# Kernel tuning notes

Measured on AMD Instinct MI355X. Metric: run time of the kernel, lower is better.

The kernel has to match this reference:

```python
import jax, jax.numpy as jnp
import numpy as np

INPUT_SIZE, HIDDEN, LEVELS = 64, 256, 2
T, B = 2048, 128


def _lstm_layer(x_seq, h0, c0, W_ih, W_hh, b_ih, b_hh):
    """Run one LSTM layer over the full sequence. x_seq: [T,B,D] -> hs: [T,B,H].
    PyTorch gate order: i, f, g, o."""
    def step(carry, x_t):
        h, c = carry
        z = x_t @ W_ih.T + b_ih + h @ W_hh.T + b_hh  # [B, 4H]
        i, f, g, o = jnp.split(z, 4, axis=-1)
        i = jax.nn.sigmoid(i)
        f = jax.nn.sigmoid(f)
        g = jnp.tanh(g)
        o = jax.nn.sigmoid(o)
        c = f * c + i * g
        h = o * jnp.tanh(c)
        return (h, c), h
    _, hs = jax.lax.scan(step, (h0, c0), x_seq)
    return hs


def setup_inputs() -> dict:
    key = jax.random.key(0)
    ks = jax.random.split(key, 16)
    s = 1.0 / np.sqrt(HIDDEN)
    inp = {
        "x": jax.random.normal(ks[0], (T, B, INPUT_SIZE), dtype=jnp.float32),
        "h0": jax.random.uniform(ks[1], (LEVELS, B, HIDDEN), dtype=jnp.float32),
        "c0": jax.random.uniform(ks[2], (LEVELS, B, HIDDEN), dtype=jnp.float32),
        # layer 0 (input -> hidden)
        "W_ih0": jax.random.uniform(ks[3], (4 * HIDDEN, INPUT_SIZE), jnp.float32, -s, s),
        "W_hh0": jax.random.uniform(ks[4], (4 * HIDDEN, HIDDEN), jnp.float32, -s, s),
        "b_ih0": jax.random.uniform(ks[5], (4 * HIDDEN,), jnp.float32, -s, s),
        "b_hh0": jax.random.uniform(ks[6], (4 * HIDDEN,), jnp.float32, -s, s),
        # layer 1 (hidden -> hidden)
        "W_ih1": jax.random.uniform(ks[7], (4 * HIDDEN, HIDDEN), jnp.float32, -s, s),
        "W_hh1": jax.random.uniform(ks[8], (4 * HIDDEN, HIDDEN), jnp.float32, -s, s),
        "b_ih1": jax.random.uniform(ks[9], (4 * HIDDEN,), jnp.float32, -s, s),
        "b_hh1": jax.random.uniform(ks[10], (4 * HIDDEN,), jnp.float32, -s, s),
        # linear head hidden -> 1
        "W_lin": jax.random.uniform(ks[11], (1, HIDDEN), jnp.float32, -s, s),
        "b_lin": jax.random.uniform(ks[12], (1,), jnp.float32, -s, s),
    }
    return inp


def reference(x, h0, c0, W_ih0, W_hh0, b_ih0, b_hh0, W_ih1, W_hh1, b_ih1, b_hh1, W_lin, b_lin):
    hs0 = _lstm_layer(x, h0[0], c0[0], W_ih0, W_hh0, b_ih0, b_hh0)   # [T,B,H]
    hs1 = _lstm_layer(hs0, h0[1], c0[1], W_ih1, W_hh1, b_ih1, b_hh1)  # [T,B,H]
    out = hs1 @ W_lin.T + b_lin  # [T,B,1]
    return out[..., 0]  # [T,B] (matches torch stack().squeeze())
```

## Files before the change

### kernel.cpp

```cpp
#include <hip/hip_runtime.h>

constexpr int TT   = 2048;
constexpr int NB   = 128;
constexpr int NI   = 64;
constexpr int NH   = 256;
constexpr int NGRP = 128;
constexpr int NWG  = 256;
constexpr int NTHR = 512;
constexpr int R0   = 8;
constexpr int R1   = 16;
constexpr int HLAG = 8;
constexpr int SLOT = (NH / 2) * NB;

__device__ unsigned g_c[64];
__device__ unsigned g_cnt = 0, g_gen = 0;

__device__ __forceinline__ float sigm(float v) { return 1.0f / (1.0f + __expf(-v)); }
__device__ __forceinline__ float tanhfast(float v) {
    float e = __expf(2.0f * v);
    return 1.0f - 2.0f / (e + 1.0f);
}
__device__ __forceinline__ float asfl(unsigned u) { return __uint_as_float(u); }
__device__ __forceinline__ unsigned f2bf(float f) {
    unsigned u = __float_as_uint(f);
    return (u + 0x7fffu + ((u >> 16) & 1u)) >> 16;
}

__device__ __forceinline__ unsigned long long ldq(const unsigned* p) {
    return __hip_atomic_load((const unsigned long long*)p, __ATOMIC_RELAXED,
                             __HIP_MEMORY_SCOPE_AGENT);
}
__device__ __forceinline__ unsigned ldd(const unsigned* p) {
    return __hip_atomic_load(p, __ATOMIC_RELAXED, __HIP_MEMORY_SCOPE_AGENT);
}
__device__ __forceinline__ void std_(unsigned* p, unsigned v) {
    __hip_atomic_store(p, v, __ATOMIC_RELAXED, __HIP_MEMORY_SCOPE_AGENT);
}
__device__ __forceinline__ void bump(unsigned* p) {
    (void)__hip_atomic_fetch_add(p, 1u, __ATOMIC_RELAXED, __HIP_MEMORY_SCOPE_AGENT);
}

__device__ __forceinline__ void pollboth(unsigned n0, unsigned n1, int lane) {
    const unsigned* p = &g_c[(lane & 1) * 32];
    for (;;) {
        unsigned v = ldd(p);
        unsigned c0v = (unsigned)__shfl((int)v, 0);
        unsigned c1v = (unsigned)__shfl((int)v, 1);
        if (c0v >= n0 && c1v >= n1) return;
        __builtin_amdgcn_s_sleep(1);
    }
}

__device__ __forceinline__ void gridbar(unsigned k, bool last) {
    __syncthreads();
    if (threadIdx.x == 0) {
        __threadfence();
        unsigned a = __hip_atomic_fetch_add(&g_cnt, 1u, __ATOMIC_ACQ_REL,
                                            __HIP_MEMORY_SCOPE_AGENT);
        if (a == k * NWG - 1u) {
            if (last) {
                __hip_atomic_store(&g_cnt, 0u, __ATOMIC_RELAXED, __HIP_MEMORY_SCOPE_AGENT);
                __hip_atomic_store(&g_gen, 0u, __ATOMIC_RELEASE, __HIP_MEMORY_SCOPE_AGENT);
            } else {
                __hip_atomic_store(&g_gen, k, __ATOMIC_RELEASE, __HIP_MEMORY_SCOPE_AGENT);
            }
        } else if (!last) {
            while (__hip_atomic_load(&g_gen, __ATOMIC_RELAXED,
                                     __HIP_MEMORY_SCOPE_AGENT) < k)
                __builtin_amdgcn_s_sleep(1);
        }
        __threadfence();
    }
    __syncthreads();
}

#define STEPQ(Q, HA, HB)                                   \
    acc[0]  += w00.Q * (HA); acc[1]  += w00.Q * (HB);      \
    acc[2]  += w01.Q * (HA); acc[3]  += w01.Q * (HB);      \
    acc[4]  += w02.Q * (HA); acc[5]  += w02.Q * (HB);      \
    acc[6]  += w03.Q * (HA); acc[7]  += w03.Q * (HB);      \
    acc[8]  += w10.Q * (HA); acc[9]  += w10.Q * (HB);      \
    acc[10] += w11.Q * (HA); acc[11] += w11.Q * (HB);      \
    acc[12] += w12.Q * (HA); acc[13] += w12.Q * (HB);      \
    acc[14] += w13.Q * (HA); acc[15] += w13.Q * (HB);

#define LOADW(W, K, kk)                                                        \
    float4 w00 = *(const float4*)((W) + (size_t)(0 * NH + j0    ) * (K) + (kk)); \
    float4 w01 = *(const float4*)((W) + (size_t)(1 * NH + j0    ) * (K) + (kk)); \
    float4 w02 = *(const float4*)((W) + (size_t)(2 * NH + j0    ) * (K) + (kk)); \
    float4 w03 = *(const float4*)((W) + (size_t)(3 * NH + j0    ) * (K) + (kk)); \
    float4 w10 = *(const float4*)((W) + (size_t)(0 * NH + j0 + 1) * (K) + (kk)); \
    float4 w11 = *(const float4*)((W) + (size_t)(1 * NH + j0 + 1) * (K) + (kk)); \
    float4 w12 = *(const float4*)((W) + (size_t)(2 * NH + j0 + 1) * (K) + (kk)); \
    float4 w13 = *(const float4*)((W) + (size_t)(3 * NH + j0 + 1) * (K) + (kk));

__device__ __forceinline__ void partH_bf(const float* __restrict__ W, int j0,
                                         int kbase,
                                         const unsigned* __restrict__ hd,
                                         int lane, float* acc) {
    const unsigned* hp = hd + (size_t)(kbase >> 1) * NB + (lane << 1);
    #pragma unroll 4
    for (int i = 0; i < 16; ++i) {
        const int kk = kbase + (i << 2);
        LOADW(W, NH, kk)
        unsigned long long q0 = ldq(hp + (size_t)(2 * i) * NB);
        unsigned long long q1 = ldq(hp + (size_t)(2 * i + 1) * NB);
        unsigned d00 = (unsigned)q0, d01 = (unsigned)(q0 >> 32);
        unsigned d10 = (unsigned)q1, d11 = (unsigned)(q1 >> 32);
        STEPQ(x, asfl(d00 << 16),          asfl(d01 << 16))
        STEPQ(y, asfl(d00 & 0xffff0000u),  asfl(d01 & 0xffff0000u))
        STEPQ(z, asfl(d10 << 16),          asfl(d11 << 16))
        STEPQ(w, asfl(d10 & 0xffff0000u),  asfl(d11 & 0xffff0000u))
    }
}

__device__ __forceinline__ void partX(const float* __restrict__ W, int j0,
                                      int k0, const float* __restrict__ xp,
                                      int lane, float* acc) {
    #pragma unroll
    for (int i4 = 0; i4 < 4; ++i4) {
        const int kk = k0 + (i4 << 2);
        LOADW(W, NI, kk)
        float4 xa = *(const float4*)(xp + (size_t)(lane << 1) * NI + kk);
        float4 xb = *(const float4*)(xp + (size_t)((lane << 1) + 1) * NI + kk);
        STEPQ(x, xa.x, xb.x)
        STEPQ(y, xa.y, xb.y)
        STEPQ(z, xa.z, xb.z)
        STEPQ(w, xa.w, xb.w)
    }
}

__global__ void __launch_bounds__(NTHR, 2) lstm2(
    const float* __restrict__ x,
    const float* __restrict__ h0in, const float* __restrict__ c0in,
    const float* __restrict__ Wih0, const float* __restrict__ Whh0,
    const float* __restrict__ bih0, const float* __restrict__ bhh0,
    const float* __restrict__ Wih1, const float* __restrict__ Whh1,
    const float* __restrict__ bih1, const float* __restrict__ bhh1,
    const float* __restrict__ Wlin, const float* __restrict__ blin,
    float* __restrict__ out,
    unsigned* __restrict__ h0d, unsigned* __restrict__ h1d)
{
    __shared__ __align__(16) float4 zp4[16 * NB];
    __shared__ float red[4];
    __shared__ unsigned go_w;

    const int tid  = threadIdx.x;
    const int gid  = blockIdx.x;
    const bool is1 = gid >= NGRP;
    const int g    = is1 ? gid - NGRP : gid;
    const int j0   = g * 2;
    const int lane = tid & 63;
    const int wv   = __builtin_amdgcn_readfirstlane(tid >> 6);

    unsigned* ownc   = is1 ? &g_c[32] : &g_c[0];

    float4 bsA = make_float4(0, 0, 0, 0), bsB = bsA;
    float cA = 0.f, cB = 0.f;
    if (tid < 128) {
        const float* bi = is1 ? bih1 : bih0;
        const float* bh = is1 ? bhh1 : bhh0;
        bsA.x = bi[0 * NH + j0] + bh[0 * NH + j0];
        bsA.y = bi[1 * NH + j0] + bh[1 * NH + j0];
        bsA.z = bi[2 * NH + j0] + bh[2 * NH + j0];
        bsA.w = bi[3 * NH + j0] + bh[3 * NH + j0];
        bsB.x = bi[0 * NH + j0 + 1] + bh[0 * NH + j0 + 1];
        bsB.y = bi[1 * NH + j0 + 1] + bh[1 * NH + j0 + 1];
        bsB.z = bi[2 * NH + j0 + 1] + bh[2 * NH + j0 + 1];
        bsB.w = bi[3 * NH + j0 + 1] + bh[3 * NH + j0 + 1];
        const float* cbase = c0in + (is1 ? 1 : 0) * NB * NH + (size_t)tid * NH + j0;
        cA = cbase[0]; cB = cbase[1];
        const float* hbase = h0in + (is1 ? 1 : 0) * NB * NH + (size_t)tid * NH + j0;
        unsigned d = (f2bf(hbase[1]) << 16) | f2bf(hbase[0]);
        unsigned* hT = is1 ? h1d : h0d;
        const int islot = is1 ? (R1 - 1) : (R0 - 1);
        std_(hT + (size_t)islot * SLOT + (size_t)g * NB + tid, d);
    }
    if (tid == 0) go_w = 0;
    const float blv = blin[0];
    asm volatile("s_waitcnt vmcnt(0)" ::: "memory");
    __syncthreads();
    if (tid == 0) bump(ownc);

    if (!is1) {
        for (int s = 0; s < TT + HLAG; ++s) {
            const unsigned tgt = (unsigned)(s + 1);
            unsigned need0 = (s < TT) ? 128u * (unsigned)(s + 1) : 0u;
            unsigned need1 = (s >= R0) ? 128u * (unsigned)(s - R0 + 2) : 0u;
            if (wv == 0) {
                pollboth(need0, need1, lane);
                if (lane == 0)
                    __hip_atomic_store(&go_w, tgt, __ATOMIC_RELAXED,
                                       __HIP_MEMORY_SCOPE_WORKGROUP);
            } else {
                while (__hip_atomic_load(&go_w, __ATOMIC_RELAXED,
                                         __HIP_MEMORY_SCOPE_WORKGROUP) < tgt) {}
            }

            if (s < TT) {
                float acc[16] = {0,0,0,0,0,0,0,0,0,0,0,0,0,0,0,0};
                if (wv < 4)
                    partH_bf(Whh0, j0, wv * 64,
                             h0d + (size_t)((s + R0 - 1) & (R0 - 1)) * SLOT, lane, acc);
                else
                    partX(Wih0, j0, (wv - 4) * 16, x + (size_t)s * NB * NI, lane, acc);
                const int base0 = ((wv << 1) + 0) * NB + (lane << 1);
                const int base1 = ((wv << 1) + 1) * NB + (lane << 1);
                zp4[base0]     = make_float4(acc[0],  acc[2],  acc[4],  acc[6]);
                zp4[base0 + 1] = make_float4(acc[1],  acc[3],  acc[5],  acc[7]);
                zp4[base1]     = make_float4(acc[8],  acc[10], acc[12], acc[14]);
                zp4[base1 + 1] = make_float4(acc[9],  acc[11], acc[13], acc[15]);
            }
            if (s >= HLAG && tid >= 256) {
                const int u = s - HLAG;
                const int k = tid - 256;
                unsigned d = ldd(h1d + (size_t)(u & (R1 - 1)) * SLOT
                                 + (size_t)(k >> 1) * NB + g);
                float hv = (k & 1) ? asfl(d & 0xffff0000u) : asfl(d << 16);
                float p = Wlin[k] * hv;
                #pragma unroll
                for (int off = 32; off; off >>= 1) p += __shfl_down(p, off);
                if (lane == 0) red[wv - 4] = p;
            }
            __syncthreads();

            if (s < TT && tid < 128) {
                float4 zA = bsA, zB = bsB;
                #pragma unroll
                for (int q = 0; q < 8; ++q) {
                    float4 a = zp4[(q * 2 + 0) * NB + tid];
                    float4 b = zp4[(q * 2 + 1) * NB + tid];
                    zA.x += a.x; zA.y += a.y; zA.z += a.z; zA.w += a.w;
                    zB.x += b.x; zB.y += b.y; zB.z += b.z; zB.w += b.w;
                }
                float iA = sigm(zA.x), fA = sigm(zA.y), gA = tanhfast(zA.z), oA = sigm(zA.w);
                cA = fA * cA + iA * gA;
                float hA = oA * tanhfast(cA);
                float iB = sigm(zB.x), fB = sigm(zB.y), gB = tanhfast(zB.z), oB = sigm(zB.w);
                cB = fB * cB + iB * gB;
                float hB = oB * tanhfast(cB);
                unsigned d = (f2bf(hB) << 16) | f2bf(hA);
                std_(h0d + (size_t)(s & (R0 - 1)) * SLOT + (size_t)g * NB + tid, d);
            }
            if (s >= HLAG && tid == 256)
                out[(size_t)(s - HLAG) * NB + g] = red[0] + red[1] + red[2] + red[3] + blv;

            asm volatile("s_waitcnt vmcnt(0)" ::: "memory");
            __syncthreads();
            if (s < TT && tid == 0) bump(&g_c[0]);
        }
    } else {
        for (int t = 0; t < TT; ++t) {
            const unsigned tgt = (unsigned)(t + 1);
            unsigned need0 = 128u * (unsigned)(t + 2);
            unsigned need1 = 128u * (unsigned)(t + 1);
            if (wv == 0) {
                pollboth(need0, need1, lane);
                if (lane == 0)
                    __hip_atomic_store(&go_w, tgt, __ATOMIC_RELAXED,
                                       __HIP_MEMORY_SCOPE_WORKGROUP);
            } else {
                while (__hip_atomic_load(&go_w, __ATOMIC_RELAXED,
                                         __HIP_MEMORY_SCOPE_WORKGROUP) < tgt) {}
            }

            float acc[16] = {0,0,0,0,0,0,0,0,0,0,0,0,0,0,0,0};
            if (wv < 4)
                partH_bf(Wih1, j0, wv * 64,
                         h0d + (size_t)(t & (R0 - 1)) * SLOT, lane, acc);
            else
                partH_bf(Whh1, j0, (wv - 4) * 64,
                         h1d + (size_t)((t + R1 - 1) & (R1 - 1)) * SLOT, lane, acc);
            const int base0 = ((wv << 1) + 0) * NB + (lane << 1);
            const int base1 = ((wv << 1) + 1) * NB + (lane << 1);
            zp4[base0]     = make_float4(acc[0],  acc[2],  acc[4],  acc[6]);
            zp4[base0 + 1] = make_float4(acc[1],  acc[3],  acc[5],  acc[7]);
            zp4[base1]     = make_float4(acc[8],  acc[10], acc[12], acc[14]);
            zp4[base1 + 1] = make_float4(acc[9],  acc[11], acc[13], acc[15]);
            __syncthreads();

            if (tid < 128) {
                float4 zA = bsA, zB = bsB;
                #pragma unroll
                for (int q = 0; q < 8; ++q) {
                    float4 a = zp4[(q * 2 + 0) * NB + tid];
                    float4 b = zp4[(q * 2 + 1) * NB + tid];
                    zA.x += a.x; zA.y += a.y; zA.z += a.z; zA.w += a.w;
                    zB.x += b.x; zB.y += b.y; zB.z += b.z; zB.w += b.w;
                }
                float iA = sigm(zA.x), fA = sigm(zA.y), gA = tanhfast(zA.z), oA = sigm(zA.w);
                cA = fA * cA + iA * gA;
                float hA = oA * tanhfast(cA);
                float iB = sigm(zB.x), fB = sigm(zB.y), gB = tanhfast(zB.z), oB = sigm(zB.w);
                cB = fB * cB + iB * gB;
                float hB = oB * tanhfast(cB);
                unsigned d = (f2bf(hB) << 16) | f2bf(hA);
                std_(h1d + (size_t)(t & (R1 - 1)) * SLOT + (size_t)g * NB + tid, d);
            }
            asm volatile("s_waitcnt vmcnt(0)" ::: "memory");
            __syncthreads();
            if (tid == 0) bump(&g_c[32]);
        }
    }

    gridbar(1, false);
    if (gid == 0 && tid == 0) {
        __hip_atomic_store(&g_c[0],  0u, __ATOMIC_RELAXED, __HIP_MEMORY_SCOPE_AGENT);
        __hip_atomic_store(&g_c[32], 0u, __ATOMIC_RELAXED, __HIP_MEMORY_SCOPE_AGENT);
    }
    gridbar(2, true);
}

extern "C" void kernel_launch(void* const* d_in, const int* in_sizes, int n_in,
                              void* d_out, int out_size, void* d_ws, size_t ws_size,
                              hipStream_t stream)
{
    const float* x    = (const float*)d_in[0];
    const float* h0in = (const float*)d_in[1];
    const float* c0in = (const float*)d_in[2];
    const float* Wih0 = (const float*)d_in[3];
    const float* Whh0 = (const float*)d_in[4];
    const float* bih0 = (const float*)d_in[5];
    const float* bhh0 = (const float*)d_in[6];
    const float* Wih1 = (const float*)d_in[7];
    const float* Whh1 = (const float*)d_in[8];
    const float* bih1 = (const float*)d_in[9];
    const float* bhh1 = (const float*)d_in[10];
    const float* Wlin = (const float*)d_in[11];
    const float* blin = (const float*)d_in[12];
    float* out = (float*)d_out;

    unsigned* h0d = (unsigned*)d_ws;
    unsigned* h1d = h0d + (size_t)R0 * SLOT;

    void* args[] = { &x, &h0in, &c0in, &Wih0, &Whh0, &bih0, &bhh0,
                     &Wih1, &Whh1, &bih1, &bhh1, &Wlin, &blin,
                     &out, &h0d, &h1d };
    hipLaunchCooperativeKernel((void*)lstm2, dim3(NWG), dim3(NTHR), args, 0, stream);
}
```

Measured before the change: 22.24 ms.

## Split per-step waits so input projection runs before waiting on recurrent state

Each workgroup now waits in two phases per step. It first computes the part that does not depend on the latest recurrent h: the x projection for layer 0, or the layer-0 hidden input for layer 1. Only then does it poll for its own layer's previous h and compute the recurrent part. Work is redistributed so all 8 waves do an equal slice of each matmul rather than half the waves per operand. This hides part of the inter-workgroup latency behind independent work, at the cost of an extra workgroup-level handoff per step.

```diff
diff --git a/kernel.cpp b/kernel.cpp
--- a/kernel.cpp
+++ b/kernel.cpp
@@ -40,13 +40,10 @@
     (void)__hip_atomic_fetch_add(p, 1u, __ATOMIC_RELAXED, __HIP_MEMORY_SCOPE_AGENT);
 }
 
-__device__ __forceinline__ void pollboth(unsigned n0, unsigned n1, int lane) {
-    const unsigned* p = &g_c[(lane & 1) * 32];
+__device__ __forceinline__ void poll1(const unsigned* p, unsigned n) {
     for (;;) {
         unsigned v = ldd(p);
-        unsigned c0v = (unsigned)__shfl((int)v, 0);
-        unsigned c1v = (unsigned)__shfl((int)v, 1);
-        if (c0v >= n0 && c1v >= n1) return;
+        if (__all(v >= n)) return;
         __builtin_amdgcn_s_sleep(1);
     }
 }
@@ -94,13 +91,13 @@
     float4 w12 = *(const float4*)((W) + (size_t)(2 * NH + j0 + 1) * (K) + (kk)); \
     float4 w13 = *(const float4*)((W) + (size_t)(3 * NH + j0 + 1) * (K) + (kk));
 
-__device__ __forceinline__ void partH_bf(const float* __restrict__ W, int j0,
-                                         int kbase,
-                                         const unsigned* __restrict__ hd,
-                                         int lane, float* acc) {
+__device__ __forceinline__ void partH32(const float* __restrict__ W, int j0,
+                                        int kbase,
+                                        const unsigned* __restrict__ hd,
+                                        int lane, float* acc) {
     const unsigned* hp = hd + (size_t)(kbase >> 1) * NB + (lane << 1);
     #pragma unroll 4
-    for (int i = 0; i < 16; ++i) {
+    for (int i = 0; i < 8; ++i) {
         const int kk = kbase + (i << 2);
         LOADW(W, NH, kk)
         unsigned long long q0 = ldq(hp + (size_t)(2 * i) * NB);
@@ -114,11 +111,11 @@
     }
 }
 
-__device__ __forceinline__ void partX(const float* __restrict__ W, int j0,
-                                      int k0, const float* __restrict__ xp,
-                                      int lane, float* acc) {
+__device__ __forceinline__ void partX8(const float* __restrict__ W, int j0,
+                                       int k0, const float* __restrict__ xp,
+                                       int lane, float* acc) {
     #pragma unroll
-    for (int i4 = 0; i4 < 4; ++i4) {
+    for (int i4 = 0; i4 < 2; ++i4) {
         const int kk = k0 + (i4 << 2);
         LOADW(W, NI, kk)
         float4 xa = *(const float4*)(xp + (size_t)(lane << 1) * NI + kk);
@@ -153,7 +150,7 @@
     const int lane = tid & 63;
     const int wv   = __builtin_amdgcn_readfirstlane(tid >> 6);
 
-    unsigned* ownc   = is1 ? &g_c[32] : &g_c[0];
+    unsigned* ownc = is1 ? &g_c[32] : &g_c[0];
 
     float4 bsA = make_float4(0, 0, 0, 0), bsB = bsA;
     float cA = 0.f, cB = 0.f;
@@ -184,33 +181,22 @@
 
     if (!is1) {
         for (int s = 0; s < TT + HLAG; ++s) {
-            const unsigned tgt = (unsigned)(s + 1);
-            unsigned need0 = (s < TT) ? 128u * (unsigned)(s + 1) : 0u;
-            unsigned need1 = (s >= R0) ? 128u * (unsigned)(s - R0 + 2) : 0u;
+            const unsigned gA = 2u * (unsigned)s + 1u;
+            const unsigned gB = gA + 1u;
             if (wv == 0) {
-                pollboth(need0, need1, lane);
+                if (s >= R0) poll1(&g_c[32], 128u * (unsigned)(s - R0 + 2));
                 if (lane == 0)
-                    __hip_atomic_store(&go_w, tgt, __ATOMIC_RELAXED,
+                    __hip_atomic_store(&go_w, gA, __ATOMIC_RELAXED,
                                        __HIP_MEMORY_SCOPE_WORKGROUP);
             } else {
                 while (__hip_atomic_load(&go_w, __ATOMIC_RELAXED,
-                                         __HIP_MEMORY_SCOPE_WORKGROUP) < tgt) {}
-            }
-
-            if (s < TT) {
-                float acc[16] = {0,0,0,0,0,0,0,0,0,0,0,0,0,0,0,0};
-                if (wv < 4)
-                    partH_bf(Whh0, j0, wv * 64,
-                             h0d + (size_t)((s + R0 - 1) & (R0 - 1)) * SLOT, lane, acc);
-                else
-                    partX(Wih0, j0, (wv - 4) * 16, x + (size_t)s * NB * NI, lane, acc);
-                const int base0 = ((wv << 1) + 0) * NB + (lane << 1);
-                const int base1 = ((wv << 1) + 1) * NB + (lane << 1);
-                zp4[base0]     = make_float4(acc[0],  acc[2],  acc[4],  acc[6]);
-                zp4[base0 + 1] = make_float4(acc[1],  acc[3],  acc[5],  acc[7]);
-                zp4[base1]     = make_float4(acc[8],  acc[10], acc[12], acc[14]);
-                zp4[base1 + 1] = make_float4(acc[9],  acc[11], acc[13], acc[15]);
-            }
+                                         __HIP_MEMORY_SCOPE_WORKGROUP) < gA) {}
+            }
+
+            float acc[16] = {0,0,0,0,0,0,0,0,0,0,0,0,0,0,0,0};
+            if (s < TT)
+                partX8(Wih0, j0, wv * 8, x + (size_t)s * NB * NI, lane, acc);
+
             if (s >= HLAG && tid >= 256) {
                 const int u = s - HLAG;
                 const int k = tid - 256;
@@ -222,6 +208,26 @@
                 for (int off = 32; off; off >>= 1) p += __shfl_down(p, off);
                 if (lane == 0) red[wv - 4] = p;
             }
+
+            if (s < TT) {
+                if (wv == 0) {
+                    poll1(&g_c[0], 128u * (unsigned)(s + 1));
+                    if (lane == 0)
+                        __hip_atomic_store(&go_w, gB, __ATOMIC_RELAXED,
+                                           __HIP_MEMORY_SCOPE_WORKGROUP);
+                } else {
+                    while (__hip_atomic_load(&go_w, __ATOMIC_RELAXED,
+                                             __HIP_MEMORY_SCOPE_WORKGROUP) < gB) {}
+                }
+                partH32(Whh0, j0, wv * 32,
+                        h0d + (size_t)((s + R0 - 1) & (R0 - 1)) * SLOT, lane, acc);
+                const int base0 = ((wv << 1) + 0) * NB + (lane << 1);
+                const int base1 = ((wv << 1) + 1) * NB + (lane << 1);
+                zp4[base0]     = make_float4(acc[0],  acc[2],  acc[4],  acc[6]);
+                zp4[base0 + 1] = make_float4(acc[1],  acc[3],  acc[5],  acc[7]);
+                zp4[base1]     = make_float4(acc[8],  acc[10], acc[12], acc[14]);
+                zp4[base1 + 1] = make_float4(acc[9],  acc[11], acc[13], acc[15]);
+            }
             __syncthreads();
 
             if (s < TT && tid < 128) {
@@ -233,11 +239,11 @@
                     zA.x += a.x; zA.y += a.y; zA.z += a.z; zA.w += a.w;
                     zB.x += b.x; zB.y += b.y; zB.z += b.z; zB.w += b.w;
                 }
-                float iA = sigm(zA.x), fA = sigm(zA.y), gA = tanhfast(zA.z), oA = sigm(zA.w);
-                cA = fA * cA + iA * gA;
+                float iA = sigm(zA.x), fA = sigm(zA.y), gA2 = tanhfast(zA.z), oA = sigm(zA.w);
+                cA = fA * cA + iA * gA2;
                 float hA = oA * tanhfast(cA);
-                float iB = sigm(zB.x), fB = sigm(zB.y), gB = tanhfast(zB.z), oB = sigm(zB.w);
-                cB = fB * cB + iB * gB;
+                float iB = sigm(zB.x), fB = sigm(zB.y), gB2 = tanhfast(zB.z), oB = sigm(zB.w);
+                cB = fB * cB + iB * gB2;
                 float hB = oB * tanhfast(cB);
                 unsigned d = (f2bf(hB) << 16) | f2bf(hA);
                 std_(h0d + (size_t)(s & (R0 - 1)) * SLOT + (size_t)g * NB + tid, d);
@@ -251,26 +257,33 @@
         }
     } else {
         for (int t = 0; t < TT; ++t) {
-            const unsigned tgt = (unsigned)(t + 1);
-            unsigned need0 = 128u * (unsigned)(t + 2);
-            unsigned need1 = 128u * (unsigned)(t + 1);
+            const unsigned gA = 2u * (unsigned)t + 1u;
+            const unsigned gB = gA + 1u;
             if (wv == 0) {
-                pollboth(need0, need1, lane);
+                poll1(&g_c[0], 128u * (unsigned)(t + 2));
                 if (lane == 0)
-                    __hip_atomic_store(&go_w, tgt, __ATOMIC_RELAXED,
+                    __hip_atomic_store(&go_w, gA, __ATOMIC_RELAXED,
                                        __HIP_MEMORY_SCOPE_WORKGROUP);
             } else {
                 while (__hip_atomic_load(&go_w, __ATOMIC_RELAXED,
-                                         __HIP_MEMORY_SCOPE_WORKGROUP) < tgt) {}
+                                         __HIP_MEMORY_SCOPE_WORKGROUP) < gA) {}
             }
 
             float acc[16] = {0,0,0,0,0,0,0,0,0,0,0,0,0,0,0,0};
-            if (wv < 4)
-                partH_bf(Wih1, j0, wv * 64,
-                         h0d + (size_t)(t & (R0 - 1)) * SLOT, lane, acc);
-            else
-                partH_bf(Whh1, j0, (wv - 4) * 64,
-                         h1d + (size_t)((t + R1 - 1) & (R1 - 1)) * SLOT, lane, acc);
+            partH32(Wih1, j0, wv * 32,
+                    h0d + (size_t)(t & (R0 - 1)) * SLOT, lane, acc);
+
+            if (wv == 0) {
+                poll1(&g_c[32], 128u * (unsigned)(t + 1));
+                if (lane == 0)
+                    __hip_atomic_store(&go_w, gB, __ATOMIC_RELAXED,
+                                       __HIP_MEMORY_SCOPE_WORKGROUP);
+            } else {
+                while (__hip_atomic_load(&go_w, __ATOMIC_RELAXED,
+                                         __HIP_MEMORY_SCOPE_WORKGROUP) < gB) {}
+            }
+            partH32(Whh1, j0, wv * 32,
+                    h1d + (size_t)((t + R1 - 1) & (R1 - 1)) * SLOT, lane, acc);
             const int base0 = ((wv << 1) + 0) * NB + (lane << 1);
             const int base1 = ((wv << 1) + 1) * NB + (lane << 1);
             zp4[base0]     = make_float4(acc[0],  acc[2],  acc[4],  acc[6]);
@@ -288,11 +301,11 @@
                     zA.x += a.x; zA.y += a.y; zA.z += a.z; zA.w += a.w;
                     zB.x += b.x; zB.y += b.y; zB.z += b.z; zB.w += b.w;
                 }
-                float iA = sigm(zA.x), fA = sigm(zA.y), gA = tanhfast(zA.z), oA = sigm(zA.w);
-                cA = fA * cA + iA * gA;
+                float iA = sigm(zA.x), fA = sigm(zA.y), gA2 = tanhfast(zA.z), oA = sigm(zA.w);
+                cA = fA * cA + iA * gA2;
                 float hA = oA * tanhfast(cA);
-                float iB = sigm(zB.x), fB = sigm(zB.y), gB = tanhfast(zB.z), oB = sigm(zB.w);
-                cB = fB * cB + iB * gB;
+                float iB = sigm(zB.x), fB = sigm(zB.y), gB2 = tanhfast(zB.z), oB = sigm(zB.w);
+                cB = fB * cB + iB * gB2;
                 float hB = oB * tanhfast(cB);
                 unsigned d = (f2bf(hB) << 16) | f2bf(hA);
                 std_(h1d + (size_t)(t & (R1 - 1)) * SLOT + (size_t)g * NB + tid, d);
```

Result: faster. 20.34 ms (median of 2 runs) (-8.5%).
